# Optimization experiments

Hardware: AMD Instinct MI355X
Metric: run time of the kernel (lower is better)

The kernel has to match this reference:

```python
import jax, jax.numpy as jnp
import numpy as np

N_NODES = 50000
N_EDGES = 1600000
D_IN = 128
D_HID = 128
D_OUT = 128


def setup_inputs() -> dict:
    key = jax.random.key(0)
    k = jax.random.split(key, 6)
    feat = jax.random.normal(k[0], (N_NODES, D_IN), dtype=jnp.float32)
    W1 = jax.random.normal(k[1], (D_IN, D_HID), dtype=jnp.float32) * (1.0 / np.sqrt(D_IN))
    b1 = jnp.zeros((D_HID,), dtype=jnp.float32)
    W2 = jax.random.normal(k[2], (D_HID, D_OUT), dtype=jnp.float32) * (1.0 / np.sqrt(D_HID))
    b2 = jnp.zeros((D_OUT,), dtype=jnp.float32)
    src = jax.random.randint(k[3], (N_EDGES,), 0, N_NODES, dtype=jnp.int32)
    dst = jax.random.randint(k[4], (N_EDGES,), 0, N_NODES, dtype=jnp.int32)
    return {"feat": feat, "W1": W1, "b1": b1, "W2": W2, "b2": b2, "src": src, "dst": dst}


def _graph_conv(h, W, b, src, dst, norm_src, norm_dst, n_nodes):
    # DGL GraphConv, norm='both': h_src * out_deg^-1/2 -> sum over edges -> * in_deg^-1/2 -> W, +b
    h = h * norm_src[:, None]
    agg = jax.ops.segment_sum(h[src], dst, num_segments=n_nodes)
    agg = agg * norm_dst[:, None]
    return agg @ W + b


def reference(feat, W1, b1, W2, b2, src, dst):
    n = feat.shape[0]
    # dgl.add_self_loop: append (i, i) for every node
    loop = jnp.arange(n, dtype=src.dtype)
    src = jnp.concatenate([src, loop])
    dst = jnp.concatenate([dst, loop])
    ones = jnp.ones(src.shape[0], dtype=feat.dtype)
    out_deg = jax.ops.segment_sum(ones, src, num_segments=n)  # >= 1 due to self-loops
    in_deg = jax.ops.segment_sum(ones, dst, num_segments=n)
    norm_src = jax.lax.rsqrt(out_deg)
    norm_dst = jax.lax.rsqrt(in_deg)
    h = _graph_conv(feat, W1, b1, src, dst, norm_src, norm_dst, n)
    h = jax.nn.relu(h)
    h = _graph_conv(h, W2, b2, src, dst, norm_src, norm_dst, n)
    return h[None, :, :]  # unsqueeze(0) -> [1, N, out_features]
```

## Files before the change

### kernel.cpp

```cpp
#include <hip/hip_runtime.h>

#define D 128
#define RANGES 4
#define CHUNKS 64
#define BINS_MAX 12512

typedef unsigned short u16;


__device__ __forceinline__ u16 f2bf(float x) {
  unsigned u = __float_as_uint(x);
  u += 0x7fffu + ((u >> 16) & 1u);
  return (u16)(u >> 16);
}
#define BF_LO(u) __uint_as_float((u) << 16)
#define BF_HI(u) __uint_as_float((u) & 0xffff0000u)


__global__ __launch_bounds__(1024)
void hist_kernel(const int* __restrict__ keys, u16* __restrict__ part,
                 int E, int N, int binsR, int chunkE)
{
  __shared__ int hist[BINS_MAX];
  const int b = blockIdx.x;
  const int r = b & (RANGES - 1);
  const int k = b >> 2;
  const int lo = r * binsR;
  const int hi = min(N, lo + binsR);
  const int nb = hi - lo;
  for (int i = threadIdx.x; i < nb; i += 1024) hist[i] = 0;
  __syncthreads();
  const int e0 = k * chunkE;
  const int e1 = min(E, e0 + chunkE);
  for (int e = e0 + threadIdx.x; e < e1; e += 1024) {
    int v = keys[e];
    if (v >= lo && v < hi) atomicAdd(&hist[v - lo], 1);
  }
  __syncthreads();
  for (int i = threadIdx.x; i < nb; i += 1024)
    part[(size_t)k * N + lo + i] = (u16)hist[i];
}

__global__ void reduce_kernel(const u16* __restrict__ psrc, u16* __restrict__ pdst,
                              int* __restrict__ deg_in, float* __restrict__ nsrc,
                              float* __restrict__ ndst, int N)
{
  int bin = blockIdx.x * blockDim.x + threadIdx.x;
  if (bin >= N) return;
  int runs = 0, rund = 0;
  for (int k = 0; k < CHUNKS; ++k) {
    runs += psrc[(size_t)k * N + bin];
    int vd = pdst[(size_t)k * N + bin];
    pdst[(size_t)k * N + bin] = (u16)rund;
    rund += vd;
  }
  deg_in[bin] = rund;
  nsrc[bin] = rsqrtf((float)runs + 1.0f);
  ndst[bin] = rsqrtf((float)rund + 1.0f);
}


__global__ __launch_bounds__(1024)
void scan1_kernel(const int* __restrict__ din, int* __restrict__ roff,
                  int* __restrict__ bsum, int N)
{
  __shared__ int wsum[16];
  const int t = threadIdx.x, lane = t & 63, wid = t >> 6;
  const int i = blockIdx.x * 1024 + t;
  int v = (i < N) ? din[i] : 0;
  int x = v;
  #pragma unroll
  for (int off = 1; off < 64; off <<= 1) {
    int u = __shfl_up(x, off);
    if (lane >= off) x += u;
  }
  if (lane == 63) wsum[wid] = x;
  __syncthreads();
  if (wid == 0) {
    int y = (lane < 16) ? wsum[lane] : 0;
    int z = y;
    #pragma unroll
    for (int off = 1; off < 16; off <<= 1) {
      int u = __shfl_up(z, off);
      if (lane >= off) z += u;
    }
    if (lane < 16) wsum[lane] = z - y;
    if (lane == 15) bsum[blockIdx.x] = z;
  }
  __syncthreads();
  if (i < N) roff[i] = wsum[wid] + (x - v);
}

__global__ void scan2_kernel(int* __restrict__ bsum, int* __restrict__ roffN, int nb)
{
  const int t = threadIdx.x;
  int v = (t < nb) ? bsum[t] : 0;
  int x = v;
  #pragma unroll
  for (int off = 1; off < 64; off <<= 1) {
    int u = __shfl_up(x, off);
    if (t >= off) x += u;
  }
  if (t < nb) bsum[t] = x - v;
  if (t == 63) *roffN = x;
}

__global__ __launch_bounds__(1024)
void scan3_kernel(int* __restrict__ roff, const int* __restrict__ bsum, int N)
{
  const int i = blockIdx.x * 1024 + threadIdx.x;
  if (i < N) roff[i] += bsum[i >> 10];
}


__global__ __launch_bounds__(1024)
void scatter_kernel(const int* __restrict__ src, const int* __restrict__ dst,
                    const u16* __restrict__ pdst, const int* __restrict__ roff,
                    u16* __restrict__ eout, int E, int N, int binsR, int chunkE)
{
  __shared__ int cur[BINS_MAX];
  const int b = blockIdx.x;
  const int r = b & (RANGES - 1);
  const int k = b >> 2;
  const int lo = r * binsR;
  const int hi = min(N, lo + binsR);
  const int nb = hi - lo;
  for (int i = threadIdx.x; i < nb; i += 1024)
    cur[i] = roff[lo + i] + (int)pdst[(size_t)k * N + lo + i];
  __syncthreads();
  const int e0 = k * chunkE;
  const int e1 = min(E, e0 + chunkE);
  for (int e = e0 + threadIdx.x; e < e1; e += 1024) {
    int d = dst[e];
    if (d >= lo && d < hi) eout[atomicAdd(&cur[d - lo], 1)] = (u16)src[e];
  }
}


__global__ __launch_bounds__(256)
void convert_kernel(const float* __restrict__ f, const float* __restrict__ nsrc,
                    unsigned* __restrict__ fb, int n4)
{
  const int i = blockIdx.x * blockDim.x + threadIdx.x;
  if (i < n4) {
    float s = nsrc[i >> 5];
    float4 v = ((const float4*)f)[i];
    uint2 o;
    o.x = (unsigned)f2bf(v.x * s) | ((unsigned)f2bf(v.y * s) << 16);
    o.y = (unsigned)f2bf(v.z * s) | ((unsigned)f2bf(v.w * s) << 16);
    ((uint2*)fb)[i] = o;
  }
}


__global__ __launch_bounds__(256)
void gather_bf_kernel(const unsigned* __restrict__ fb, const u16* __restrict__ eidx,
                      const int* __restrict__ roff, const float* __restrict__ ndst,
                      u16* __restrict__ outb, int N)
{
  const int wid = threadIdx.x >> 6;
  const int lane = threadIdx.x & 63;
  const int node = blockIdx.x * 4 + wid;
  if (node >= N) return;
  const int h = lane >> 5;
  const int q = lane & 31;
  const uint2* fb2 = (const uint2*)fb;
  float4 acc = make_float4(0.f, 0.f, 0.f, 0.f);
  if (h == 0) {
    uint2 u = fb2[(size_t)node * 32 + q];
    acc.x = BF_LO(u.x); acc.y = BF_HI(u.x);
    acc.z = BF_LO(u.y); acc.w = BF_HI(u.y);
  }
  const int beg = roff[node], end = roff[node + 1];
  for (int e0 = beg; e0 < end; e0 += 64) {
    const int cnt = min(64, end - e0);
    int id = (lane < cnt) ? (int)eidx[e0 + lane] : 0;
    int j = 0;
    for (; j + 16 <= cnt; j += 16) {
      int s0 = __shfl(id, j + 0 + h);
      int s1 = __shfl(id, j + 2 + h);
      int s2 = __shfl(id, j + 4 + h);
      int s3 = __shfl(id, j + 6 + h);
      int s4 = __shfl(id, j + 8 + h);
      int s5 = __shfl(id, j + 10 + h);
      int s6 = __shfl(id, j + 12 + h);
      int s7 = __shfl(id, j + 14 + h);
      uint2 u0 = fb2[(size_t)s0 * 32 + q];
      uint2 u1 = fb2[(size_t)s1 * 32 + q];
      uint2 u2 = fb2[(size_t)s2 * 32 + q];
      uint2 u3 = fb2[(size_t)s3 * 32 + q];
      uint2 u4 = fb2[(size_t)s4 * 32 + q];
      uint2 u5 = fb2[(size_t)s5 * 32 + q];
      uint2 u6 = fb2[(size_t)s6 * 32 + q];
      uint2 u7 = fb2[(size_t)s7 * 32 + q];
      acc.x += BF_LO(u0.x); acc.y += BF_HI(u0.x); acc.z += BF_LO(u0.y); acc.w += BF_HI(u0.y);
      acc.x += BF_LO(u1.x); acc.y += BF_HI(u1.x); acc.z += BF_LO(u1.y); acc.w += BF_HI(u1.y);
      acc.x += BF_LO(u2.x); acc.y += BF_HI(u2.x); acc.z += BF_LO(u2.y); acc.w += BF_HI(u2.y);
      acc.x += BF_LO(u3.x); acc.y += BF_HI(u3.x); acc.z += BF_LO(u3.y); acc.w += BF_HI(u3.y);
      acc.x += BF_LO(u4.x); acc.y += BF_HI(u4.x); acc.z += BF_LO(u4.y); acc.w += BF_HI(u4.y);
      acc.x += BF_LO(u5.x); acc.y += BF_HI(u5.x); acc.z += BF_LO(u5.y); acc.w += BF_HI(u5.y);
      acc.x += BF_LO(u6.x); acc.y += BF_HI(u6.x); acc.z += BF_LO(u6.y); acc.w += BF_HI(u6.y);
      acc.x += BF_LO(u7.x); acc.y += BF_HI(u7.x); acc.z += BF_LO(u7.y); acc.w += BF_HI(u7.y);
    }
    for (; j < cnt; j += 2) {
      int ej = j + h;
      int s = __shfl(id, ej & 63);
      if (ej < cnt) {
        uint2 u = fb2[(size_t)s * 32 + q];
        acc.x += BF_LO(u.x); acc.y += BF_HI(u.x);
        acc.z += BF_LO(u.y); acc.w += BF_HI(u.y);
      }
    }
  }
  acc.x += __shfl_xor(acc.x, 32);
  acc.y += __shfl_xor(acc.y, 32);
  acc.z += __shfl_xor(acc.z, 32);
  acc.w += __shfl_xor(acc.w, 32);
  if (h == 0) {
    float nd = ndst[node];
    ushort4 w;
    w.x = f2bf(acc.x * nd); w.y = f2bf(acc.y * nd);
    w.z = f2bf(acc.z * nd); w.w = f2bf(acc.w * nd);
    *(ushort4*)(outb + (size_t)node * D + q * 4) = w;
  }
}


template<bool RELU_SCALE, bool BF_OUT>
__global__ __launch_bounds__(256)
void gemm128(const u16* __restrict__ A, const float* __restrict__ W,
             const float* __restrict__ bias, const float* __restrict__ nsrc,
             void* __restrict__ Cv, int N)
{
  __shared__ float As[64][36];
  __shared__ float Bs[32][128];
  const int t = threadIdx.x;
  const int tx = t & 15;
  const int ty = t >> 4;
  const int r0 = blockIdx.x * 64;
  float acc[4][8];
  #pragma unroll
  for (int j = 0; j < 4; ++j)
    #pragma unroll
    for (int cc = 0; cc < 8; ++cc) acc[j][cc] = 0.f;

  for (int kc = 0; kc < D; kc += 32) {
    __syncthreads();
    {
      int q2 = t * 2;
      int row = q2 >> 3;
      int fc = q2 & 7;
      int gr = r0 + row; if (gr > N - 1) gr = N - 1;
      uint4 u = *(const uint4*)(A + (size_t)gr * D + kc + fc * 4);
      float4 f0 = make_float4(BF_LO(u.x), BF_HI(u.x), BF_LO(u.y), BF_HI(u.y));
      float4 f1 = make_float4(BF_LO(u.z), BF_HI(u.z), BF_LO(u.w), BF_HI(u.w));
      *(float4*)(&As[row][fc * 4]) = f0;
      *(float4*)(&As[row][fc * 4 + 4]) = f1;
    }
    #pragma unroll
    for (int m = 0; m < 4; ++m) {
      int q = t + 256 * m;
      int kk = q >> 5;
      int fc = q & 31;
      float4 v = *(const float4*)(W + (size_t)(kc + kk) * D + fc * 4);
      *(float4*)(&Bs[kk][fc * 4]) = v;
    }
    __syncthreads();
    #pragma unroll
    for (int k = 0; k < 32; ++k) {
      float a0 = As[ty * 4 + 0][k];
      float a1 = As[ty * 4 + 1][k];
      float a2 = As[ty * 4 + 2][k];
      float a3 = As[ty * 4 + 3][k];
      float4 bv0 = *(const float4*)(&Bs[k][tx * 4]);
      float4 bv1 = *(const float4*)(&Bs[k][64 + tx * 4]);
      float bb[8] = {bv0.x, bv0.y, bv0.z, bv0.w, bv1.x, bv1.y, bv1.z, bv1.w};
      #pragma unroll
      for (int cc = 0; cc < 8; ++cc) {
        acc[0][cc] += a0 * bb[cc];
        acc[1][cc] += a1 * bb[cc];
        acc[2][cc] += a2 * bb[cc];
        acc[3][cc] += a3 * bb[cc];
      }
    }
  }

  float4 bb0 = *(const float4*)(bias + tx * 4);
  float4 bb1 = *(const float4*)(bias + 64 + tx * 4);
  float bb[8] = {bb0.x, bb0.y, bb0.z, bb0.w, bb1.x, bb1.y, bb1.z, bb1.w};
  #pragma unroll
  for (int j = 0; j < 4; ++j) {
    int gr = r0 + ty * 4 + j;
    if (gr < N) {
      float s = RELU_SCALE ? nsrc[gr] : 1.0f;
      float o[8];
      #pragma unroll
      for (int cc = 0; cc < 8; ++cc) {
        float v = acc[j][cc] + bb[cc];
        if (RELU_SCALE) v = fmaxf(v, 0.f) * s;
        o[cc] = v;
      }
      if (BF_OUT) {
        u16* Cb = (u16*)Cv;
        ushort4 w0, w1;
        w0.x = f2bf(o[0]); w0.y = f2bf(o[1]); w0.z = f2bf(o[2]); w0.w = f2bf(o[3]);
        w1.x = f2bf(o[4]); w1.y = f2bf(o[5]); w1.z = f2bf(o[6]); w1.w = f2bf(o[7]);
        *(ushort4*)(Cb + (size_t)gr * D + tx * 4) = w0;
        *(ushort4*)(Cb + (size_t)gr * D + 64 + tx * 4) = w1;
      } else {
        float* C = (float*)Cv;
        *(float4*)(C + (size_t)gr * D + tx * 4) = make_float4(o[0], o[1], o[2], o[3]);
        *(float4*)(C + (size_t)gr * D + 64 + tx * 4) = make_float4(o[4], o[5], o[6], o[7]);
      }
    }
  }
}


extern "C" void kernel_launch(void* const* d_in, const int* in_sizes, int n_in,
                              void* d_out, int out_size, void* d_ws, size_t ws_size,
                              hipStream_t stream) {
  const float* feat = (const float*)d_in[0];
  const float* W1   = (const float*)d_in[1];
  const float* b1   = (const float*)d_in[2];
  const float* W2   = (const float*)d_in[3];
  const float* b2   = (const float*)d_in[4];
  const int*   src  = (const int*)d_in[5];
  const int*   dst  = (const int*)d_in[6];
  const int N = in_sizes[0] / D;
  const int E = in_sizes[5];
  float* out = (float*)d_out;

  const int binsR = (N + RANGES - 1) / RANGES;
  const int chunkE = (((E + CHUNKS - 1) / CHUNKS) + 3) & ~3;

  auto align256 = [](size_t x) { return (x + 255) & ~(size_t)255; };
  char* p = (char*)d_ws;
  char* p0 = p;  p += align256((size_t)CHUNKS * N * 2);
  char* p1 = p;  p += align256((size_t)N * D * 2);
  char* p2 = p;  p += align256((size_t)N * D * 2);
  int*   deg_in  = (int*)p;   p += align256((size_t)N * 4);
  int*   row_off = (int*)p;   p += align256((size_t)(N + 1) * 4);
  float* nsrc    = (float*)p; p += align256((size_t)N * 4);
  float* ndst    = (float*)p; p += align256((size_t)N * 4);
  int*   bsum    = (int*)p;   p += 256;

  u16*      psrc   = (u16*)p0;
  u16*      esrc   = (u16*)p0;
  u16*      pdst   = (u16*)p1;
  u16*      h1bf   = (u16*)p1;
  unsigned* featbf = (unsigned*)p2;
  u16*      agg2   = (u16*)p2;
  u16*      agg1   = (u16*)((char*)d_out + (size_t)N * D * 2);

  const int nblk = (N + 1023) / 1024;

  hist_kernel<<<RANGES * CHUNKS, 1024, 0, stream>>>(src, psrc, E, N, binsR, chunkE);
  hist_kernel<<<RANGES * CHUNKS, 1024, 0, stream>>>(dst, pdst, E, N, binsR, chunkE);
  reduce_kernel<<<(N + 255) / 256, 256, 0, stream>>>(psrc, pdst, deg_in, nsrc, ndst, N);
  convert_kernel<<<(N * D / 4 + 255) / 256, 256, 0, stream>>>(feat, nsrc, featbf, N * D / 4);
  scan1_kernel<<<nblk, 1024, 0, stream>>>(deg_in, row_off, bsum, N);
  scan2_kernel<<<1, 64, 0, stream>>>(bsum, row_off + N, nblk);
  scan3_kernel<<<nblk, 1024, 0, stream>>>(row_off, bsum, N);
  scatter_kernel<<<RANGES * CHUNKS, 1024, 0, stream>>>(src, dst, pdst, row_off, esrc, E, N, binsR, chunkE);

  gather_bf_kernel<<<(N + 3) / 4, 256, 0, stream>>>(featbf, esrc, row_off, ndst, agg1, N);
  gemm128<true, true><<<(N + 63) / 64, 256, 0, stream>>>(agg1, W1, b1, nsrc, h1bf, N);
  gather_bf_kernel<<<(N + 3) / 4, 256, 0, stream>>>((const unsigned*)h1bf, esrc, row_off, ndst, agg2, N);
  gemm128<false, false><<<(N + 63) / 64, 256, 0, stream>>>(agg2, W2, b2, nsrc, out, N);
}
```

Measured before the change: 306.5 us.

## Replace FP32 LDS-tiled GEMMs with bf16 MFMA kernels using pre-transposed weights

Both dense 128x128 projections move from a scalar FP32 shared-memory tiled GEMM to a per-wave 16-row tile computed with the 16x16x32 bf16 MFMA intrinsic. A new small kernel converts W1 and W2 to bf16 and transposes them so each lane can load contiguous K-slices of B straight from global memory. This removes LDS staging and barriers and cuts ALU work, but it also rounds the weights to bf16 and writes outputs as scattered scalar stores rather than vector stores.

After: 297.5 us. -2.9%, faster.

```diff
diff --git a/kernel.cpp b/kernel.cpp
--- a/kernel.cpp
+++ b/kernel.cpp
@@ -6,6 +6,8 @@
 #define BINS_MAX 12512
 
 typedef unsigned short u16;
+typedef __attribute__((ext_vector_type(8))) short short8;
+typedef __attribute__((ext_vector_type(4))) float f32x4;
 
 
 __device__ __forceinline__ u16 f2bf(float x) {
@@ -150,6 +152,18 @@
     o.y = (unsigned)f2bf(v.z * s) | ((unsigned)f2bf(v.w * s) << 16);
     ((uint2*)fb)[i] = o;
   }
+}
+
+
+__global__ __launch_bounds__(128)
+void wtrans_kernel(const float* __restrict__ W1, const float* __restrict__ W2,
+                   u16* __restrict__ Wt1, u16* __restrict__ Wt2)
+{
+  const int k = blockIdx.x & 127;
+  const float* W = (blockIdx.x < 128) ? W1 : W2;
+  u16* Wt = (blockIdx.x < 128) ? Wt1 : Wt2;
+  const int n = threadIdx.x;
+  Wt[n * 128 + k] = f2bf(W[k * 128 + n]);
 }
 
 
@@ -228,89 +242,47 @@
 
 template<bool RELU_SCALE, bool BF_OUT>
 __global__ __launch_bounds__(256)
-void gemm128(const u16* __restrict__ A, const float* __restrict__ W,
-             const float* __restrict__ bias, const float* __restrict__ nsrc,
-             void* __restrict__ Cv, int N)
-{
-  __shared__ float As[64][36];
-  __shared__ float Bs[32][128];
-  const int t = threadIdx.x;
-  const int tx = t & 15;
-  const int ty = t >> 4;
-  const int r0 = blockIdx.x * 64;
-  float acc[4][8];
-  #pragma unroll
-  for (int j = 0; j < 4; ++j)
+void gemm_mfma(const u16* __restrict__ A, const u16* __restrict__ Wt,
+               const float* __restrict__ bias, const float* __restrict__ nsrc,
+               void* __restrict__ Cv, int N)
+{
+  const int lane = threadIdx.x & 63;
+  const int wv   = threadIdx.x >> 6;
+  const int tile = blockIdx.x * 4 + wv;
+  if (tile * 16 >= N) return;
+  const int m  = lane & 15;
+  const int kb = lane >> 4;
+  int arow = tile * 16 + m; if (arow > N - 1) arow = N - 1;
+  f32x4 acc[8];
+  #pragma unroll
+  for (int c = 0; c < 8; ++c) acc[c] = (f32x4){0.f, 0.f, 0.f, 0.f};
+  #pragma unroll
+  for (int kc = 0; kc < D; kc += 32) {
+    short8 a = *(const short8*)(A + (size_t)arow * D + kc + kb * 8);
     #pragma unroll
-    for (int cc = 0; cc < 8; ++cc) acc[j][cc] = 0.f;
-
-  for (int kc = 0; kc < D; kc += 32) {
-    __syncthreads();
-    {
-      int q2 = t * 2;
-      int row = q2 >> 3;
-      int fc = q2 & 7;
-      int gr = r0 + row; if (gr > N - 1) gr = N - 1;
-      uint4 u = *(const uint4*)(A + (size_t)gr * D + kc + fc * 4);
-      float4 f0 = make_float4(BF_LO(u.x), BF_HI(u.x), BF_LO(u.y), BF_HI(u.y));
-      float4 f1 = make_float4(BF_LO(u.z), BF_HI(u.z), BF_LO(u.w), BF_HI(u.w));
-      *(float4*)(&As[row][fc * 4]) = f0;
-      *(float4*)(&As[row][fc * 4 + 4]) = f1;
-    }
+    for (int c = 0; c < 8; ++c) {
+      short8 b = *(const short8*)(Wt + (size_t)(c * 16 + m) * D + kc + kb * 8);
+      acc[c] = __builtin_amdgcn_mfma_f32_16x16x32_bf16(a, b, acc[c], 0, 0, 0);
+    }
+  }
+  float ns[4];
+  #pragma unroll
+  for (int j = 0; j < 4; ++j) {
+    int orow = tile * 16 + kb * 4 + j;
+    ns[j] = (RELU_SCALE && orow < N) ? nsrc[orow] : 1.0f;
+  }
+  #pragma unroll
+  for (int c = 0; c < 8; ++c) {
+    const int col = c * 16 + m;
+    const float bb = bias[col];
     #pragma unroll
-    for (int m = 0; m < 4; ++m) {
-      int q = t + 256 * m;
-      int kk = q >> 5;
-      int fc = q & 31;
-      float4 v = *(const float4*)(W + (size_t)(kc + kk) * D + fc * 4);
-      *(float4*)(&Bs[kk][fc * 4]) = v;
-    }
-    __syncthreads();
-    #pragma unroll
-    for (int k = 0; k < 32; ++k) {
-      float a0 = As[ty * 4 + 0][k];
-      float a1 = As[ty * 4 + 1][k];
-      float a2 = As[ty * 4 + 2][k];
-      float a3 = As[ty * 4 + 3][k];
-      float4 bv0 = *(const float4*)(&Bs[k][tx * 4]);
-      float4 bv1 = *(const float4*)(&Bs[k][64 + tx * 4]);
-      float bb[8] = {bv0.x, bv0.y, bv0.z, bv0.w, bv1.x, bv1.y, bv1.z, bv1.w};
-      #pragma unroll
-      for (int cc = 0; cc < 8; ++cc) {
-        acc[0][cc] += a0 * bb[cc];
-        acc[1][cc] += a1 * bb[cc];
-        acc[2][cc] += a2 * bb[cc];
-        acc[3][cc] += a3 * bb[cc];
-      }
-    }
-  }
-
-  float4 bb0 = *(const float4*)(bias + tx * 4);
-  float4 bb1 = *(const float4*)(bias + 64 + tx * 4);
-  float bb[8] = {bb0.x, bb0.y, bb0.z, bb0.w, bb1.x, bb1.y, bb1.z, bb1.w};
-  #pragma unroll
-  for (int j = 0; j < 4; ++j) {
-    int gr = r0 + ty * 4 + j;
-    if (gr < N) {
-      float s = RELU_SCALE ? nsrc[gr] : 1.0f;
-      float o[8];
-      #pragma unroll
-      for (int cc = 0; cc < 8; ++cc) {
-        float v = acc[j][cc] + bb[cc];
-        if (RELU_SCALE) v = fmaxf(v, 0.f) * s;
-        o[cc] = v;
-      }
-      if (BF_OUT) {
-        u16* Cb = (u16*)Cv;
-        ushort4 w0, w1;
-        w0.x = f2bf(o[0]); w0.y = f2bf(o[1]); w0.z = f2bf(o[2]); w0.w = f2bf(o[3]);
-        w1.x = f2bf(o[4]); w1.y = f2bf(o[5]); w1.z = f2bf(o[6]); w1.w = f2bf(o[7]);
-        *(ushort4*)(Cb + (size_t)gr * D + tx * 4) = w0;
-        *(ushort4*)(Cb + (size_t)gr * D + 64 + tx * 4) = w1;
-      } else {
-        float* C = (float*)Cv;
-        *(float4*)(C + (size_t)gr * D + tx * 4) = make_float4(o[0], o[1], o[2], o[3]);
-        *(float4*)(C + (size_t)gr * D + 64 + tx * 4) = make_float4(o[4], o[5], o[6], o[7]);
+    for (int j = 0; j < 4; ++j) {
+      int orow = tile * 16 + kb * 4 + j;
+      if (orow < N) {
+        float v = acc[c][j] + bb;
+        if (RELU_SCALE) v = fmaxf(v, 0.f) * ns[j];
+        if (BF_OUT) ((u16*)Cv)[(size_t)orow * D + col] = f2bf(v);
+        else        ((float*)Cv)[(size_t)orow * D + col] = v;
       }
     }
   }
@@ -344,6 +316,8 @@
   float* nsrc    = (float*)p; p += align256((size_t)N * 4);
   float* ndst    = (float*)p; p += align256((size_t)N * 4);
   int*   bsum    = (int*)p;   p += 256;
+  u16*   wt1     = (u16*)p;   p += align256((size_t)D * D * 2);
+  u16*   wt2     = (u16*)p;   p += align256((size_t)D * D * 2);
 
   u16*      psrc   = (u16*)p0;
   u16*      esrc   = (u16*)p0;
@@ -354,7 +328,9 @@
   u16*      agg1   = (u16*)((char*)d_out + (size_t)N * D * 2);
 
   const int nblk = (N + 1023) / 1024;
-
+  const int gemm_grid = ((N + 15) / 16 + 3) / 4;
+
+  wtrans_kernel<<<256, 128, 0, stream>>>(W1, W2, wt1, wt2);
   hist_kernel<<<RANGES * CHUNKS, 1024, 0, stream>>>(src, psrc, E, N, binsR, chunkE);
   hist_kernel<<<RANGES * CHUNKS, 1024, 0, stream>>>(dst, pdst, E, N, binsR, chunkE);
   reduce_kernel<<<(N + 255) / 256, 256, 0, stream>>>(psrc, pdst, deg_in, nsrc, ndst, N);
@@ -365,7 +341,7 @@
   scatter_kernel<<<RANGES * CHUNKS, 1024, 0, stream>>>(src, dst, pdst, row_off, esrc, E, N, binsR, chunkE);
 
   gather_bf_kernel<<<(N + 3) / 4, 256, 0, stream>>>(featbf, esrc, row_off, ndst, agg1, N);
-  gemm128<true, true><<<(N + 63) / 64, 256, 0, stream>>>(agg1, W1, b1, nsrc, h1bf, N);
+  gemm_mfma<true, true><<<gemm_grid, 256, 0, stream>>>(agg1, wt1, b1, nsrc, h1bf, N);
   gather_bf_kernel<<<(N + 3) / 4, 256, 0, stream>>>((const unsigned*)h1bf, esrc, row_off, ndst, agg2, N);
-  gemm128<false, false><<<(N + 63) / 64, 256, 0, stream>>>(agg2, W2, b2, nsrc, out, N);
-}
+  gemm_mfma<false, false><<<gemm_grid, 256, 0, stream>>>(agg2, wt2, b2, nsrc, out, N);
+}
```
